# Kernel optimization log

Hardware: AMD Instinct MI355X
Metric: run time of the kernel (lower is better)

Reference implementation:

```python
import jax, jax.numpy as jnp
import numpy as np

N_NODES = 100_000
N_EDGES = 3_200_000
N_FEAT = 128
HIDDEN = 16
OUT = 2
N_GRAPHS = 64


def setup_inputs() -> dict:
    key = jax.random.key(0)
    ks = jax.random.split(key, 12)
    x = jax.random.normal(ks[0], (N_NODES, N_FEAT), dtype=jnp.float32)
    edge_index = jax.random.randint(ks[1], (2, N_EDGES), 0, N_NODES, dtype=jnp.int64)
    batch_idx = jnp.sort(jax.random.randint(ks[2], (N_NODES,), 0, N_GRAPHS, dtype=jnp.int64))

    def glorot(k, shape):
        s = jnp.sqrt(6.0 / (shape[0] + shape[1])).astype(jnp.float32)
        return jax.random.uniform(k, shape, jnp.float32, -1.0, 1.0) * s

    return {
        "x": x, "edge_index": edge_index, "batch_idx": batch_idx,
        "W0": glorot(ks[3], (N_FEAT, HIDDEN)), "b0": jnp.zeros((HIDDEN,), jnp.float32),
        "a0": jnp.full((1,), 0.25, jnp.float32),  # PReLU default weight
        "W1": glorot(ks[4], (HIDDEN, HIDDEN)), "b1": jnp.zeros((HIDDEN,), jnp.float32),
        "a1": jnp.full((1,), 0.25, jnp.float32),
        "W2": glorot(ks[5], (HIDDEN, HIDDEN)), "b2": jnp.zeros((HIDDEN,), jnp.float32),
        "a2": jnp.full((1,), 0.25, jnp.float32),
        "W3": glorot(ks[6], (HIDDEN, OUT)), "b3": jnp.zeros((OUT,), jnp.float32),
    }


def _prelu(x, a):
    return jnp.where(x > 0, x, a * x)


def _gcn_conv(x, W, b, src, dst, norm, n):
    # PyG GCNConv: linear transform, then normalized gather-scatter aggregation, then bias
    h = x @ W                                   # [N, out]
    msg = h[src] * norm[:, None]                # gather + per-edge scale
    out = jax.ops.segment_sum(msg, dst, num_segments=n)  # scatter-add into targets
    return out + b


def reference(x, edge_index, batch_idx, W0, b0, a0, W1, b1, a1, W2, b2, a2, W3, b3):
    n = x.shape[0]
    loop = jnp.arange(n, dtype=edge_index.dtype)
    src = jnp.concatenate([edge_index[0], loop])  # add self loops
    dst = jnp.concatenate([edge_index[1], loop])
    # symmetric degree normalization deg^-1/2 (deg over targets, all edge weights = 1)
    deg = jax.ops.segment_sum(jnp.ones_like(dst, dtype=x.dtype), dst, num_segments=n)
    dinv = jnp.where(deg > 0, jax.lax.rsqrt(deg), 0.0)
    norm = dinv[src] * dinv[dst]

    h = _prelu(_gcn_conv(x, W0, b0, src, dst, norm, n), a0)
    h = _prelu(_gcn_conv(h, W1, b1, src, dst, norm, n), a1)
    h = _prelu(_gcn_conv(h, W2, b2, src, dst, norm, n), a2)
    h = _gcn_conv(h, W3, b3, src, dst, norm, n)

    # global_mean_pool over graph ids
    sums = jax.ops.segment_sum(h, batch_idx, num_segments=N_GRAPHS)
    cnts = jax.ops.segment_sum(jnp.ones((n,), h.dtype), batch_idx, num_segments=N_GRAPHS)
    return sums / jnp.maximum(cnts, 1.0)[:, None]
```

## Files before the change

### kernel.cpp

```cpp
#include <hip/hip_runtime.h>


#define NN 100000
#define NE 3200000
#define NF 128
#define NH 16
#define NO 2
#define NG 64
#define NBLK 391
#define BN 256
#define NBUK 391
#define CHUNK 4096
#define NBLKA 782
#define CAPF 10240
#define NT0 6250

typedef __attribute__((ext_vector_type(8))) short short8;
typedef __attribute__((ext_vector_type(4))) float float4v;


__device__ __forceinline__ float ldf(const void* p, int i, int f32) {
  if (f32) return ((const float*)p)[i];
  unsigned int u = ((const unsigned short*)p)[i];
  return __uint_as_float(u << 16);
}
__device__ __forceinline__ int ldi(const void* p, int i, int i64) {
  if (i64) return (int)((const long long*)p)[i];
  return ((const int*)p)[i];
}
__device__ __forceinline__ void stf(void* p, int i, float v, int f32) {
  if (f32) {
    ((float*)p)[i] = v;
  } else {
    unsigned int w = __float_as_uint(v);
    unsigned int r = (w + 0x7fffu + ((w >> 16) & 1u)) >> 16;
    ((unsigned short*)p)[i] = (unsigned short)r;
  }
}
__device__ __forceinline__ float bf16lo(unsigned int u) { return __uint_as_float(u << 16); }
__device__ __forceinline__ float bf16hi(unsigned int u) { return __uint_as_float(u & 0xffff0000u); }
__device__ __forceinline__ unsigned int packbf(float x, float y) {
  unsigned int a = __float_as_uint(x);
  a = (a + 0x7fffu + ((a >> 16) & 1u)) >> 16;
  unsigned int b = __float_as_uint(y);
  b = (b + 0x7fffu + ((b >> 16) & 1u)) & 0xffff0000u;
  return a | b;
}
__device__ __forceinline__ int okf(float v) { return (v == v) && (fabsf(v) < 1e30f); }
__device__ __forceinline__ void nflag(int* diag, int bad, int bit) {
  if (__any(bad)) {
    if ((threadIdx.x & 63) == 0) atomicOr(diag + 2, 1 << bit);
  }
}
__device__ __forceinline__ int clampi(int v, int hi) {
  return (unsigned)v < (unsigned)hi ? v : 0;
}


__global__ __launch_bounds__(1024) void k_sniff(const void* x, const void* ei, int* zbase) {
  int tid = threadIdx.x;
  if (tid < 624) zbase[tid] = 0;
  __syncthreads();
  if (tid < 64) {
    unsigned int xv = ((const unsigned int*)x)[tid];
    unsigned int e = (xv >> 7) & 0xffu;
    int hit = (e >= 116u && e <= 133u);
    int hits = __popcll(__ballot(hit));
    unsigned int ev = ((const unsigned int*)ei)[2 * tid + 1];
    int nzc = __popcll(__ballot(ev != 0u));
    if (tid == 0) {
      zbase[0] = (hits < 32) ? 1 : 0;
      zbase[1] = (nzc == 0) ? 1 : 0;
    }
  }
}


__global__ __launch_bounds__(512) void k_build(const void* ei, const int* __restrict__ diag,
                                               int* __restrict__ cursor, int* __restrict__ ents) {
  __shared__ int spktA[CHUNK];
  __shared__ unsigned short sbid[CHUNK];
  __shared__ unsigned short srank[CHUNK];
  __shared__ int spktB[CHUNK];
  __shared__ int gpos[CHUNK];
  __shared__ int lscan[512];
  __shared__ int sexcl[NBUK];
  __shared__ int goff[NBUK];
  int tid = threadIdx.x, blk = blockIdx.x;
  lscan[tid] = 0;
  __syncthreads();
  int i64 = diag[1];
  int base = blk * CHUNK;
  int n = NE - base; n = n > CHUNK ? CHUNK : n;
  for (int i = tid; i < n; i += 512) {
    int sv = clampi(ldi(ei, base + i, i64), NN);
    int dv = clampi(ldi(ei, NE + base + i, i64), NN);
    int b = dv >> 8;
    spktA[i] = ((dv & 255) << 17) | sv;
    sbid[i] = (unsigned short)b;
    srank[i] = (unsigned short)atomicAdd(&lscan[b], 1);
  }
  __syncthreads();
  for (int off = 1; off < 512; off <<= 1) {
    int v = (tid >= off) ? lscan[tid - off] : 0;
    __syncthreads();
    lscan[tid] += v;
    __syncthreads();
  }
  if (tid < NBUK) {
    int b = tid;
    int incl = lscan[b];
    int excl = (b > 0) ? lscan[b - 1] : 0;
    int cnt = incl - excl;
    sexcl[b] = excl;
    int rbase = cnt ? atomicAdd(&cursor[b], cnt) : 0;
    goff[b] = b * CAPF + rbase - excl;
  }
  __syncthreads();
  for (int i = tid; i < n; i += 512) {
    int b = sbid[i];
    int rr = sexcl[b] + srank[i];
    spktB[rr] = spktA[i];
    int gp = goff[b] + rr;
    int hi = b * CAPF + CAPF - 1;
    gpos[rr] = gp <= hi ? gp : hi;
  }
  __syncthreads();
  for (int r = tid; r < n; r += 512) ents[gpos[r]] = spktB[r];
}

__global__ __launch_bounds__(512) void k_bsort(int* __restrict__ ents, const int* __restrict__ cursor,
                                               int* __restrict__ rowstart, int* __restrict__ rowend,
                                               float* __restrict__ dinv, int* __restrict__ diag) {
  __shared__ int ent[CAPF];
  __shared__ unsigned short rnk[CAPF];
  __shared__ int lcnt[BN];
  __shared__ int sexcl[BN];
  int tid = threadIdx.x, b = blockIdx.x;
  int bs = b * CAPF;
  int n = cursor[b];
  if (n > CAPF) { n = CAPF; if (tid == 0) atomicOr(diag + 2, 1 << 9); }
  if (tid < BN) lcnt[tid] = 0;
  __syncthreads();
  for (int i = tid; i < n; i += 512) {
    int e = ents[bs + i];
    ent[i] = e;
    rnk[i] = (unsigned short)atomicAdd(&lcnt[e >> 17], 1);
  }
  __syncthreads();
  int c = (tid < BN) ? lcnt[tid] : 0;
  for (int off = 1; off < BN; off <<= 1) {
    int v = (tid < BN && tid >= off) ? lcnt[tid - off] : 0;
    __syncthreads();
    if (tid < BN) lcnt[tid] += v;
    __syncthreads();
  }
  if (tid < BN) {
    int excl = lcnt[tid] - c;
    sexcl[tid] = excl;
    int node = (b << 8) + tid;
    if (node < NN) {
      rowstart[node] = bs + excl;
      rowend[node] = bs + excl + c;
      dinv[node] = rsqrtf((float)(c + 1));
    }
  }
  __syncthreads();
  for (int i = tid; i < n; i += 512) {
    int e = ent[i];
    ents[bs + sexcl[e >> 17] + rnk[i]] = e & 0x1FFFF;
  }
}


__global__ __launch_bounds__(256) void k_t0(const void* __restrict__ x, const void* __restrict__ W0,
                                            const float* __restrict__ dinv,
                                            int* __restrict__ diag, unsigned int* __restrict__ out) {
  __shared__ float ws[NF * NH];
  __shared__ float xs[16 * 129];
  int tid = threadIdx.x;
  int f32 = diag[0];
  if (!f32) {
    const unsigned short* xu = (const unsigned short*)x;
    const unsigned short* wu = (const unsigned short*)W0;
    int wave = tid >> 6, lane = tid & 63;
    int nfe = lane & 15, quad = lane >> 4;
    short8 bfr[4];
#pragma unroll
    for (int mf = 0; mf < 4; ++mf) {
      short8 t;
#pragma unroll
      for (int j = 0; j < 8; ++j) t[j] = (short)wu[(mf * 32 + quad * 8 + j) * NH + nfe];
      bfr[mf] = t;
    }
    int tile = blockIdx.x * 4 + wave;
    if (tile < NT0) {
      int node0 = tile * 16;
      const short8* xrow = (const short8*)(xu + (node0 + nfe) * NF);
      float4v c = {0.f, 0.f, 0.f, 0.f};
#pragma unroll
      for (int mf = 0; mf < 4; ++mf) {
        short8 a = xrow[mf * 4 + quad];
        c = __builtin_amdgcn_mfma_f32_16x16x32_bf16(a, bfr[mf], c, 0, 0, 0);
      }
      int bad = 0;
#pragma unroll
      for (int r = 0; r < 4; ++r) {
        int node = node0 + quad * 4 + r;
        float v = c[r] * dinv[node];
        float o = __shfl_xor(v, 1);
        if (!(nfe & 1)) out[node * 8 + (nfe >> 1)] = packbf(v, o);
        bad |= !okf(v);
      }
      nflag(diag, bad, 0);
    }
  } else {
    for (int t = 0; t < 4; ++t) {
      int tile = blockIdx.x * 4 + t;
      if (tile >= NT0) break;
      int node0 = tile * 16;
      __syncthreads();
#pragma unroll
      for (int r = 0; r < 8; ++r) ws[tid + 256 * r] = ldf(W0, tid + 256 * r, 1);
#pragma unroll
      for (int r = 0; r < 8; ++r) {
        int idx = tid + 256 * r;
        int row = idx >> 7, col = idx & 127;
        xs[row * 129 + col] = ldf(x, (node0 + row) * NF + col, 1);
      }
      __syncthreads();
      int nl = tid >> 4, f = tid & 15;
      float acc = 0.f;
#pragma unroll 4
      for (int k = 0; k < NF; ++k) acc += xs[nl * 129 + k] * ws[k * NH + f];
      acc *= dinv[node0 + nl];
      float other = __shfl_xor(acc, 1);
      if ((f & 1) == 0) out[(node0 + nl) * 8 + (f >> 1)] = packbf(acc, other);
      nflag(diag, !okf(acc), 0);
    }
  }
}


__global__ __launch_bounds__(256) void k_aggT(const uint2* __restrict__ hin,
                                              const int* __restrict__ srcs,
                                              const int* __restrict__ rowstart,
                                              const int* __restrict__ rowend,
                                              const float* __restrict__ dinv,
                                              const void* __restrict__ b, const void* __restrict__ a,
                                              const void* __restrict__ Wn,
                                              int* __restrict__ diag, int bit,
                                              uint2* __restrict__ hout) {
  __shared__ float ws[NH * NH];
  int tid = threadIdx.x;
  int f32 = diag[0];
  ws[tid] = ldf(Wn, tid, f32);
  __syncthreads();
  int gid = blockIdx.x * 256 + tid;
  if (gid >= NN * 4) return;
  int node = gid >> 2, p = gid & 3;
  uint2 self = hin[gid];
  float acc0 = bf16lo(self.x), acc1 = bf16hi(self.x);
  float acc2 = bf16lo(self.y), acc3 = bf16hi(self.y);
  int e = rowstart[node], e1 = rowend[node];
  for (; e + 8 <= e1; e += 8) {
    uint2 v[8];
#pragma unroll
    for (int k = 0; k < 8; ++k) v[k] = hin[srcs[e + k] * 4 + p];
#pragma unroll
    for (int k = 0; k < 8; ++k) {
      acc0 += bf16lo(v[k].x);
      acc1 += bf16hi(v[k].x);
      acc2 += bf16lo(v[k].y);
      acc3 += bf16hi(v[k].y);
    }
  }
  for (; e + 2 <= e1; e += 2) {
    uint2 va = hin[srcs[e] * 4 + p];
    uint2 vb = hin[srcs[e + 1] * 4 + p];
    acc0 += bf16lo(va.x) + bf16lo(vb.x);
    acc1 += bf16hi(va.x) + bf16hi(vb.x);
    acc2 += bf16lo(va.y) + bf16lo(vb.y);
    acc3 += bf16hi(va.y) + bf16hi(vb.y);
  }
  if (e < e1) {
    uint2 v = hin[srcs[e] * 4 + p];
    acc0 += bf16lo(v.x);
    acc1 += bf16hi(v.x);
    acc2 += bf16lo(v.y);
    acc3 += bf16hi(v.y);
  }
  float dv = dinv[node];
  float av = ldf(a, 0, f32);
  float p0 = dv * acc0 + ldf(b, 4 * p + 0, f32);
  float p1 = dv * acc1 + ldf(b, 4 * p + 1, f32);
  float p2 = dv * acc2 + ldf(b, 4 * p + 2, f32);
  float p3 = dv * acc3 + ldf(b, 4 * p + 3, f32);
  p0 = p0 > 0.f ? p0 : av * p0;
  p1 = p1 > 0.f ? p1 : av * p1;
  p2 = p2 > 0.f ? p2 : av * p2;
  p3 = p3 > 0.f ? p3 : av * p3;
  float t0 = 0.f, t1 = 0.f, t2 = 0.f, t3 = 0.f;
#pragma unroll
  for (int j = 0; j < 4; ++j) {
    float q0 = __shfl(p0, j, 4);
    float q1 = __shfl(p1, j, 4);
    float q2 = __shfl(p2, j, 4);
    float q3 = __shfl(p3, j, 4);
    const float* w0 = &ws[(4 * j) * NH + 4 * p];
    const float* w1 = &ws[(4 * j + 1) * NH + 4 * p];
    const float* w2 = &ws[(4 * j + 2) * NH + 4 * p];
    const float* w3 = &ws[(4 * j + 3) * NH + 4 * p];
    t0 += q0 * w0[0] + q1 * w1[0] + q2 * w2[0] + q3 * w3[0];
    t1 += q0 * w0[1] + q1 * w1[1] + q2 * w2[1] + q3 * w3[1];
    t2 += q0 * w0[2] + q1 * w1[2] + q2 * w2[2] + q3 * w3[2];
    t3 += q0 * w0[3] + q1 * w1[3] + q2 * w2[3] + q3 * w3[3];
  }
  t0 *= dv; t1 *= dv; t2 *= dv; t3 *= dv;
  uint2 o;
  o.x = packbf(t0, t1);
  o.y = packbf(t2, t3);
  hout[gid] = o;
  nflag(diag, !okf(t0) || !okf(t3), bit);
}

__global__ __launch_bounds__(256) void k_aggT3(const uint2* __restrict__ hin,
                                               const int* __restrict__ srcs,
                                               const int* __restrict__ rowstart,
                                               const int* __restrict__ rowend,
                                               const float* __restrict__ dinv,
                                               const void* __restrict__ b, const void* __restrict__ a,
                                               const void* __restrict__ W3,
                                               int* __restrict__ diag, float2* __restrict__ hout) {
  __shared__ float ws[NH * NO];
  int tid = threadIdx.x;
  int f32 = diag[0];
  if (tid < NH * NO) ws[tid] = ldf(W3, tid, f32);
  __syncthreads();
  int gid = blockIdx.x * 256 + tid;
  if (gid >= NN * 4) return;
  int node = gid >> 2, p = gid & 3;
  uint2 self = hin[gid];
  float acc0 = bf16lo(self.x), acc1 = bf16hi(self.x);
  float acc2 = bf16lo(self.y), acc3 = bf16hi(self.y);
  int e = rowstart[node], e1 = rowend[node];
  for (; e + 8 <= e1; e += 8) {
    uint2 v[8];
#pragma unroll
    for (int k = 0; k < 8; ++k) v[k] = hin[srcs[e + k] * 4 + p];
#pragma unroll
    for (int k = 0; k < 8; ++k) {
      acc0 += bf16lo(v[k].x);
      acc1 += bf16hi(v[k].x);
      acc2 += bf16lo(v[k].y);
      acc3 += bf16hi(v[k].y);
    }
  }
  for (; e + 2 <= e1; e += 2) {
    uint2 va = hin[srcs[e] * 4 + p];
    uint2 vb = hin[srcs[e + 1] * 4 + p];
    acc0 += bf16lo(va.x) + bf16lo(vb.x);
    acc1 += bf16hi(va.x) + bf16hi(vb.x);
    acc2 += bf16lo(va.y) + bf16lo(vb.y);
    acc3 += bf16hi(va.y) + bf16hi(vb.y);
  }
  if (e < e1) {
    uint2 v = hin[srcs[e] * 4 + p];
    acc0 += bf16lo(v.x);
    acc1 += bf16hi(v.x);
    acc2 += bf16lo(v.y);
    acc3 += bf16hi(v.y);
  }
  float dv = dinv[node];
  float av = ldf(a, 0, f32);
  float p0 = dv * acc0 + ldf(b, 4 * p + 0, f32);
  float p1 = dv * acc1 + ldf(b, 4 * p + 1, f32);
  float p2 = dv * acc2 + ldf(b, 4 * p + 2, f32);
  float p3 = dv * acc3 + ldf(b, 4 * p + 3, f32);
  p0 = p0 > 0.f ? p0 : av * p0;
  p1 = p1 > 0.f ? p1 : av * p1;
  p2 = p2 > 0.f ? p2 : av * p2;
  p3 = p3 > 0.f ? p3 : av * p3;
  float u0 = p0 * ws[(4 * p) * NO]     + p1 * ws[(4 * p + 1) * NO] +
             p2 * ws[(4 * p + 2) * NO] + p3 * ws[(4 * p + 3) * NO];
  float u1 = p0 * ws[(4 * p) * NO + 1]     + p1 * ws[(4 * p + 1) * NO + 1] +
             p2 * ws[(4 * p + 2) * NO + 1] + p3 * ws[(4 * p + 3) * NO + 1];
  u0 += __shfl_xor(u0, 1, 4);
  u0 += __shfl_xor(u0, 2, 4);
  u1 += __shfl_xor(u1, 1, 4);
  u1 += __shfl_xor(u1, 2, 4);
  if (p == 0) hout[node] = make_float2(dv * u0, dv * u1);
  nflag(diag, !okf(u0) || !okf(u1), 6);
}

__global__ __launch_bounds__(256) void k_agg2p(const float2* __restrict__ tin,
                                               const int* __restrict__ srcs,
                                               const int* __restrict__ rowstart,
                                               const int* __restrict__ rowend,
                                               const float* __restrict__ dinv,
                                               const void* __restrict__ b3,
                                               const void* __restrict__ batch,
                                               int* __restrict__ diag, float* __restrict__ pool) {
  __shared__ float ssum[NG * NO];
  __shared__ float scnt[NG];
  int tid = threadIdx.x;
  int f32 = diag[0], i64 = diag[1];
  if (tid < NG * NO) ssum[tid] = 0.f;
  if (tid < NG) scnt[tid] = 0.f;
  __syncthreads();
  int node = blockIdx.x * 256 + tid;
  if (node < NN) {
    float2 t = tin[node];
    float a0 = t.x, a1 = t.y;
    int e = rowstart[node], e1 = rowend[node];
    for (; e + 4 <= e1; e += 4) {
      int s0 = srcs[e], s1 = srcs[e + 1], s2 = srcs[e + 2], s3 = srcs[e + 3];
      float2 h0 = tin[s0], h1 = tin[s1], h2 = tin[s2], h3 = tin[s3];
      a0 += h0.x + h1.x + h2.x + h3.x;
      a1 += h0.y + h1.y + h2.y + h3.y;
    }
    for (; e < e1; ++e) {
      float2 hv = tin[srcs[e]];
      a0 += hv.x;
      a1 += hv.y;
    }
    float dv = dinv[node];
    a0 = dv * a0 + ldf(b3, 0, f32);
    a1 = dv * a1 + ldf(b3, 1, f32);
    int g = ldi(batch, node, i64);
    g = (unsigned)g < NG ? g : 0;
    atomicAdd(&ssum[g * 2], a0);
    atomicAdd(&ssum[g * 2 + 1], a1);
    atomicAdd(&scnt[g], 1.f);
    nflag(diag, !okf(a0) || !okf(a1), 7);
  }
  __syncthreads();
  if (tid < NG * NO && ssum[tid] != 0.f) atomicAdd(&pool[tid], ssum[tid]);
  if (tid < NG && scnt[tid] != 0.f) atomicAdd(&pool[NG * NO + tid], scnt[tid]);
}

__global__ __launch_bounds__(128) void k_final(const float* __restrict__ pool,
                                               const int* __restrict__ diag, void* __restrict__ out) {
  int i = threadIdx.x;
  int f32 = diag[0], i64 = diag[1], stg = diag[2];
  float c = pool[NG * NO + (i >> 1)];
  c = c > 1.f ? c : 1.f;
  float v = pool[i] / c;
  if (stg != 0 || !okf(v)) {
    int stage = stg ? __ffs(stg) : 15;
    v = 1024.0f + stage * 64.0f + f32 * 16.0f + i64 * 8.0f;
  }
  stf(out, i, v, f32);
}

__global__ __launch_bounds__(128) void k_diag_ws(void* out, float v) {
  unsigned int w = __float_as_uint(v);
  ((unsigned short*)out)[threadIdx.x] = (unsigned short)(w >> 16);
}


extern "C" void kernel_launch(void* const* d_in, const int* in_sizes, int n_in,
                              void* d_out, int out_size, void* d_ws, size_t ws_size,
                              hipStream_t stream) {
  const void* x  = d_in[0];
  const void* ei = d_in[1];
  const void* batch = d_in[2];
  const void* W0 = d_in[3];
  const void* b0 = d_in[4];
  const void* a0 = d_in[5];
  const void* W1 = d_in[6];
  const void* b1 = d_in[7];
  const void* a1 = d_in[8];
  const void* W2 = d_in[9];
  const void* b2 = d_in[10];
  const void* a2 = d_in[11];
  const void* W3 = d_in[12];
  const void* b3 = d_in[13];

  char* w = (char*)d_ws;
  int* diag         = (int*)(w + 0);
  float* pool       = (float*)(w + 64);
  int* cursor       = (int*)(w + 896);
  float* dinv       = (float*)(w + 2496);
  int* rowstart     = (int*)(w + 402496);
  int* rowend       = (int*)(w + 802496);
  int* ents         = (int*)(w + 1202496);
  uint2* hsA        = (uint2*)(w + 17217856);
  uint2* hsB        = (uint2*)(w + 20417856);
  float2* hs3       = (float2*)(w + 23617856);
  const size_t NEED = 24417856;

  if (ws_size < NEED) {
    k_diag_ws<<<1, 128, 0, stream>>>(d_out, (float)ws_size);
    return;
  }

  k_sniff<<<1, 1024, 0, stream>>>(x, ei, (int*)w);

  k_build<<<NBLKA, 512, 0, stream>>>(ei, diag, cursor, ents);
  k_bsort<<<NBUK, 512, 0, stream>>>(ents, cursor, rowstart, rowend, dinv, diag);

  k_t0<<<(NT0 + 3) / 4, 256, 0, stream>>>(x, W0, dinv, diag, (unsigned int*)hsA);
  k_aggT<<<(NN * 4 + 255) / 256, 256, 0, stream>>>(hsA, ents, rowstart, rowend, dinv, b0, a0, W1, diag, 1, hsB);
  k_aggT<<<(NN * 4 + 255) / 256, 256, 0, stream>>>(hsB, ents, rowstart, rowend, dinv, b1, a1, W2, diag, 3, hsA);
  k_aggT3<<<(NN * 4 + 255) / 256, 256, 0, stream>>>(hsA, ents, rowstart, rowend, dinv, b2, a2, W3, diag, hs3);
  k_agg2p<<<NBLK, 256, 0, stream>>>(hs3, ents, rowstart, rowend, dinv, b3, batch, diag, pool);

  k_final<<<1, 128, 0, stream>>>(pool, diag, d_out);
}
```

Measured before the change: 302.2 us.

## Pack CSR row start/count, halve build chunk, fuse final into pooling kernel

Halves the edge-bucketing chunk size and doubles its block count to raise occupancy. The intermediate gpos array is dropped, and the bucket sort now writes to a separate buffer using atomic cursors instead of staging the bucket in LDS. rowstart and rowend are packed into one 32-bit word holding a 22-bit offset and a 10-bit count, so each aggregation reads one index load per node. The final normalization kernel is removed; the last pooling block finishes the work through a done counter, saving one launch at the cost of extra atomics and a degree cap of 1023.

After: 313.9 us. 1.04x slower.

```diff
diff --git a/kernel.cpp b/kernel.cpp
--- a/kernel.cpp
+++ b/kernel.cpp
@@ -10,8 +10,8 @@
 #define NBLK 391
 #define BN 256
 #define NBUK 391
-#define CHUNK 4096
-#define NBLKA 782
+#define CHUNK 2048
+#define NBLKA 1563
 #define CAPF 10240
 #define NT0 6250
 
@@ -57,9 +57,9 @@
 }
 
 
-__global__ __launch_bounds__(1024) void k_sniff(const void* x, const void* ei, int* zbase) {
+__global__ __launch_bounds__(1024) void k_zero(const void* x, const void* ei, int* zbase) {
   int tid = threadIdx.x;
-  if (tid < 624) zbase[tid] = 0;
+  if (tid < 640) zbase[tid] = 0;
   __syncthreads();
   if (tid < 64) {
     unsigned int xv = ((const unsigned int*)x)[tid];
@@ -76,13 +76,13 @@
 }
 
 
-__global__ __launch_bounds__(512) void k_build(const void* ei, const int* __restrict__ diag,
-                                               int* __restrict__ cursor, int* __restrict__ ents) {
+__global__ __launch_bounds__(512, 5) void k_build(const void* ei, const int* __restrict__ diag,
+                                                  int* __restrict__ cursor, int* __restrict__ ents) {
   __shared__ int spktA[CHUNK];
   __shared__ unsigned short sbid[CHUNK];
   __shared__ unsigned short srank[CHUNK];
   __shared__ int spktB[CHUNK];
-  __shared__ int gpos[CHUNK];
+  __shared__ unsigned short sbidB[CHUNK];
   __shared__ int lscan[512];
   __shared__ int sexcl[NBUK];
   __shared__ int goff[NBUK];
@@ -108,45 +108,41 @@
     __syncthreads();
   }
   if (tid < NBUK) {
-    int b = tid;
-    int incl = lscan[b];
-    int excl = (b > 0) ? lscan[b - 1] : 0;
+    int incl = lscan[tid];
+    int excl = (tid > 0) ? lscan[tid - 1] : 0;
     int cnt = incl - excl;
-    sexcl[b] = excl;
-    int rbase = cnt ? atomicAdd(&cursor[b], cnt) : 0;
-    goff[b] = b * CAPF + rbase - excl;
+    sexcl[tid] = excl;
+    int rbase = cnt ? atomicAdd(&cursor[tid], cnt) : 0;
+    goff[tid] = tid * CAPF + rbase - excl;
   }
   __syncthreads();
   for (int i = tid; i < n; i += 512) {
     int b = sbid[i];
     int rr = sexcl[b] + srank[i];
     spktB[rr] = spktA[i];
-    int gp = goff[b] + rr;
+    sbidB[rr] = (unsigned short)b;
+  }
+  __syncthreads();
+  for (int r = tid; r < n; r += 512) {
+    int b = sbidB[r];
+    int gp = goff[b] + r;
     int hi = b * CAPF + CAPF - 1;
-    gpos[rr] = gp <= hi ? gp : hi;
-  }
-  __syncthreads();
-  for (int r = tid; r < n; r += 512) ents[gpos[r]] = spktB[r];
-}
-
-__global__ __launch_bounds__(512) void k_bsort(int* __restrict__ ents, const int* __restrict__ cursor,
-                                               int* __restrict__ rowstart, int* __restrict__ rowend,
+    ents[gp <= hi ? gp : hi] = spktB[r];
+  }
+}
+
+__global__ __launch_bounds__(512) void k_bsort(const int* __restrict__ ents, const int* __restrict__ cursor,
+                                               int* __restrict__ ents2, unsigned int* __restrict__ rsc,
                                                float* __restrict__ dinv, int* __restrict__ diag) {
-  __shared__ int ent[CAPF];
-  __shared__ unsigned short rnk[CAPF];
   __shared__ int lcnt[BN];
-  __shared__ int sexcl[BN];
+  __shared__ int lcur[BN];
   int tid = threadIdx.x, b = blockIdx.x;
   int bs = b * CAPF;
   int n = cursor[b];
   if (n > CAPF) { n = CAPF; if (tid == 0) atomicOr(diag + 2, 1 << 9); }
   if (tid < BN) lcnt[tid] = 0;
   __syncthreads();
-  for (int i = tid; i < n; i += 512) {
-    int e = ents[bs + i];
-    ent[i] = e;
-    rnk[i] = (unsigned short)atomicAdd(&lcnt[e >> 17], 1);
-  }
+  for (int i = tid; i < n; i += 512) atomicAdd(&lcnt[ents[bs + i] >> 17], 1);
   __syncthreads();
   int c = (tid < BN) ? lcnt[tid] : 0;
   for (int off = 1; off < BN; off <<= 1) {
@@ -157,18 +153,20 @@
   }
   if (tid < BN) {
     int excl = lcnt[tid] - c;
-    sexcl[tid] = excl;
+    lcur[tid] = excl;
     int node = (b << 8) + tid;
     if (node < NN) {
-      rowstart[node] = bs + excl;
-      rowend[node] = bs + excl + c;
+      int cc = c > 1023 ? 1023 : c;
+      rsc[node] = (unsigned int)(bs + excl) | ((unsigned int)cc << 22);
       dinv[node] = rsqrtf((float)(c + 1));
+      if (c > 1023) atomicOr(diag + 2, 1 << 10);
     }
   }
   __syncthreads();
   for (int i = tid; i < n; i += 512) {
-    int e = ent[i];
-    ents[bs + sexcl[e >> 17] + rnk[i]] = e & 0x1FFFF;
+    int e = ents[bs + i];
+    int r = atomicAdd(&lcur[e >> 17], 1);
+    ents2[bs + r] = e & 0x1FFFF;
   }
 }
 
@@ -244,8 +242,7 @@
 
 __global__ __launch_bounds__(256) void k_aggT(const uint2* __restrict__ hin,
                                               const int* __restrict__ srcs,
-                                              const int* __restrict__ rowstart,
-                                              const int* __restrict__ rowend,
+                                              const unsigned int* __restrict__ rsc,
                                               const float* __restrict__ dinv,
                                               const void* __restrict__ b, const void* __restrict__ a,
                                               const void* __restrict__ Wn,
@@ -262,7 +259,9 @@
   uint2 self = hin[gid];
   float acc0 = bf16lo(self.x), acc1 = bf16hi(self.x);
   float acc2 = bf16lo(self.y), acc3 = bf16hi(self.y);
-  int e = rowstart[node], e1 = rowend[node];
+  unsigned int rv = rsc[node];
+  int e = (int)(rv & 0x3FFFFFu);
+  int e1 = e + (int)(rv >> 22);
   for (; e + 8 <= e1; e += 8) {
     uint2 v[8];
 #pragma unroll
@@ -326,8 +325,7 @@
 
 __global__ __launch_bounds__(256) void k_aggT3(const uint2* __restrict__ hin,
                                                const int* __restrict__ srcs,
-                                               const int* __restrict__ rowstart,
-                                               const int* __restrict__ rowend,
+                                               const unsigned int* __restrict__ rsc,
                                                const float* __restrict__ dinv,
                                                const void* __restrict__ b, const void* __restrict__ a,
                                                const void* __restrict__ W3,
@@ -343,7 +341,9 @@
   uint2 self = hin[gid];
   float acc0 = bf16lo(self.x), acc1 = bf16hi(self.x);
   float acc2 = bf16lo(self.y), acc3 = bf16hi(self.y);
-  int e = rowstart[node], e1 = rowend[node];
+  unsigned int rv = rsc[node];
+  int e = (int)(rv & 0x3FFFFFu);
+  int e1 = e + (int)(rv >> 22);
   for (; e + 8 <= e1; e += 8) {
     uint2 v[8];
 #pragma unroll
@@ -395,14 +395,15 @@
 
 __global__ __launch_bounds__(256) void k_agg2p(const float2* __restrict__ tin,
                                                const int* __restrict__ srcs,
-                                               const int* __restrict__ rowstart,
-                                               const int* __restrict__ rowend,
+                                               const unsigned int* __restrict__ rsc,
                                                const float* __restrict__ dinv,
                                                const void* __restrict__ b3,
                                                const void* __restrict__ batch,
-                                               int* __restrict__ diag, float* __restrict__ pool) {
+                                               int* __restrict__ diag, float* __restrict__ pool,
+                                               int* __restrict__ done, void* __restrict__ out) {
   __shared__ float ssum[NG * NO];
   __shared__ float scnt[NG];
+  __shared__ int islast;
   int tid = threadIdx.x;
   int f32 = diag[0], i64 = diag[1];
   if (tid < NG * NO) ssum[tid] = 0.f;
@@ -412,7 +413,9 @@
   if (node < NN) {
     float2 t = tin[node];
     float a0 = t.x, a1 = t.y;
-    int e = rowstart[node], e1 = rowend[node];
+    unsigned int rv = rsc[node];
+    int e = (int)(rv & 0x3FFFFFu);
+    int e1 = e + (int)(rv >> 22);
     for (; e + 4 <= e1; e += 4) {
       int s0 = srcs[e], s1 = srcs[e + 1], s2 = srcs[e + 2], s3 = srcs[e + 3];
       float2 h0 = tin[s0], h1 = tin[s1], h2 = tin[s2], h3 = tin[s3];
@@ -437,20 +440,27 @@
   __syncthreads();
   if (tid < NG * NO && ssum[tid] != 0.f) atomicAdd(&pool[tid], ssum[tid]);
   if (tid < NG && scnt[tid] != 0.f) atomicAdd(&pool[NG * NO + tid], scnt[tid]);
-}
-
-__global__ __launch_bounds__(128) void k_final(const float* __restrict__ pool,
-                                               const int* __restrict__ diag, void* __restrict__ out) {
-  int i = threadIdx.x;
-  int f32 = diag[0], i64 = diag[1], stg = diag[2];
-  float c = pool[NG * NO + (i >> 1)];
-  c = c > 1.f ? c : 1.f;
-  float v = pool[i] / c;
-  if (stg != 0 || !okf(v)) {
-    int stage = stg ? __ffs(stg) : 15;
-    v = 1024.0f + stage * 64.0f + f32 * 16.0f + i64 * 8.0f;
-  }
-  stf(out, i, v, f32);
+  __syncthreads();
+  if (tid == 0) {
+    __threadfence();
+    int old = atomicAdd(done, 1);
+    islast = (old == NBLK - 1);
+  }
+  __syncthreads();
+  if (!islast) return;
+  __threadfence();
+  if (tid < NG * NO) {
+    float s = atomicAdd(&pool[tid], 0.f);
+    float c = atomicAdd(&pool[NG * NO + (tid >> 1)], 0.f);
+    c = c > 1.f ? c : 1.f;
+    float v = s / c;
+    int stg = atomicOr(diag + 2, 0);
+    if (stg != 0 || !okf(v)) {
+      int stage = stg ? __ffs(stg) : 15;
+      v = 1024.0f + stage * 64.0f + f32 * 16.0f + i64 * 8.0f;
+    }
+    stf(out, tid, v, f32);
+  }
 }
 
 __global__ __launch_bounds__(128) void k_diag_ws(void* out, float v) {
@@ -480,31 +490,30 @@
   char* w = (char*)d_ws;
   int* diag         = (int*)(w + 0);
   float* pool       = (float*)(w + 64);
+  int* done         = (int*)(w + 832);
   int* cursor       = (int*)(w + 896);
-  float* dinv       = (float*)(w + 2496);
-  int* rowstart     = (int*)(w + 402496);
-  int* rowend       = (int*)(w + 802496);
-  int* ents         = (int*)(w + 1202496);
-  uint2* hsA        = (uint2*)(w + 17217856);
-  uint2* hsB        = (uint2*)(w + 20417856);
-  float2* hs3       = (float2*)(w + 23617856);
-  const size_t NEED = 24417856;
+  float* dinv       = (float*)(w + 2560);
+  unsigned int* rsc = (unsigned int*)(w + 402560);
+  int* ents         = (int*)(w + 802560);
+  int* ents2        = (int*)(w + 16817920);
+  uint2* hsA        = (uint2*)(w + 32833280);
+  uint2* hsB        = (uint2*)(w + 36033280);
+  float2* hs3       = (float2*)(w + 39233280);
+  const size_t NEED = 40033280;
 
   if (ws_size < NEED) {
     k_diag_ws<<<1, 128, 0, stream>>>(d_out, (float)ws_size);
     return;
   }
 
-  k_sniff<<<1, 1024, 0, stream>>>(x, ei, (int*)w);
+  k_zero<<<1, 1024, 0, stream>>>(x, ei, (int*)w);
 
   k_build<<<NBLKA, 512, 0, stream>>>(ei, diag, cursor, ents);
-  k_bsort<<<NBUK, 512, 0, stream>>>(ents, cursor, rowstart, rowend, dinv, diag);
+  k_bsort<<<NBUK, 512, 0, stream>>>(ents, cursor, ents2, rsc, dinv, diag);
 
   k_t0<<<(NT0 + 3) / 4, 256, 0, stream>>>(x, W0, dinv, diag, (unsigned int*)hsA);
-  k_aggT<<<(NN * 4 + 255) / 256, 256, 0, stream>>>(hsA, ents, rowstart, rowend, dinv, b0, a0, W1, diag, 1, hsB);
-  k_aggT<<<(NN * 4 + 255) / 256, 256, 0, stream>>>(hsB, ents, rowstart, rowend, dinv, b1, a1, W2, diag, 3, hsA);
-  k_aggT3<<<(NN * 4 + 255) / 256, 256, 0, stream>>>(hsA, ents, rowstart, rowend, dinv, b2, a2, W3, diag, hs3);
-  k_agg2p<<<NBLK, 256, 0, stream>>>(hs3, ents, rowstart, rowend, dinv, b3, batch, diag, pool);
-
-  k_final<<<1, 128, 0, stream>>>(pool, diag, d_out);
-}
+  k_aggT<<<(NN * 4 + 255) / 256, 256, 0, stream>>>(hsA, ents2, rsc, dinv, b0, a0, W1, diag, 1, hsB);
+  k_aggT<<<(NN * 4 + 255) / 256, 256, 0, stream>>>(hsB, ents2, rsc, dinv, b1, a1, W2, diag, 3, hsA);
+  k_aggT3<<<(NN * 4 + 255) / 256, 256, 0, stream>>>(hsA, ents2, rsc, dinv, b2, a2, W3, diag, hs3);
+  k_agg2p<<<NBLK, 256, 0, stream>>>(hs3, ents2, rsc, dinv, b3, batch, diag, pool, done, d_out);
+}
```
